# Performance work log

Hardware: AMD Instinct MI355X
Metric: run time of the kernel (lower is better)

The kernel has to match this reference:

```python
import jax, jax.numpy as jnp
import numpy as np

N = 100000      # nodes
E = 1600000     # edges (avg degree 16)
F_DIM = 64      # input feature
H = 64          # hidden1
D1 = 64         # decoder1
P = 200000      # number of query pairs
EPS = 0.0       # GIN eps (train_eps=False)


def setup_inputs() -> dict:
    key = jax.random.key(0)
    ks = jax.random.split(key, 12)
    x = jax.random.normal(ks[0], (N, F_DIM), jnp.float32)
    edge_index = jax.random.randint(ks[1], (2, E), 0, N, dtype=jnp.int32)
    curvature = jax.random.normal(ks[2], (E,), jnp.float32)
    idx = jax.random.randint(ks[3], (2, P), 0, N, dtype=jnp.int32)
    s1 = 1.0 / np.sqrt(F_DIM)
    s2 = 1.0 / np.sqrt(H)
    s3 = 1.0 / np.sqrt(4 * H)
    s4 = 1.0 / np.sqrt(D1)
    w1 = jax.random.uniform(ks[4], (F_DIM, H), jnp.float32, -s1, s1)
    b1 = jax.random.uniform(ks[5], (H,), jnp.float32, -s1, s1)
    w2 = jax.random.uniform(ks[6], (H, H), jnp.float32, -s2, s2)
    b2 = jax.random.uniform(ks[7], (H,), jnp.float32, -s2, s2)
    dw1 = jax.random.uniform(ks[8], (4 * H, D1), jnp.float32, -s3, s3)
    db1 = jax.random.uniform(ks[9], (D1,), jnp.float32, -s3, s3)
    dw2 = jax.random.uniform(ks[10], (D1, 1), jnp.float32, -s4, s4)
    db2 = jax.random.uniform(ks[11], (1,), jnp.float32, -s4, s4)
    return {"x": x, "edge_index": edge_index, "curvature": curvature, "idx": idx,
            "w1": w1, "b1": b1, "w2": w2, "b2": b2,
            "dw1": dw1, "db1": db1, "dw2": dw2, "db2": db2}


def reference(x, edge_index, curvature, idx, w1, b1, w2, b2, dw1, db1, dw2, db2):
    # curvature path: abs + dropout (eval mode => identity), result unused by output
    _ = jnp.abs(curvature)
    src, dst = edge_index[0], edge_index[1]
    # GIN aggregation with self-loops of weight 1: sum_j x_j + x_i
    agg = jax.ops.segment_sum(x[src], dst, num_segments=N) + x  # [N, F]
    h = (1.0 + EPS) * x + agg
    # nn = Linear -> ReLU -> Linear
    h = jnp.maximum(h @ w1 + b1, 0.0) @ w2 + b2                 # [N, H]
    h = jnp.maximum(h, 0.0)                                     # outer ReLU
    e1 = h[idx[0]]                                              # [P, H]
    e2 = h[idx[1]]                                              # [P, H]
    feat = jnp.concatenate([e1 + e2, e1 * e2, e1, e2], axis=1)  # [P, 4H]
    log = jnp.maximum(feat @ dw1 + db1, 0.0) @ dw2 + db2        # [P, 1]
    return log
```

## Files before the change

### kernel.cpp

```cpp
#include <hip/hip_runtime.h>
#include <hip/hip_bf16.h>
#include <hip/hip_fp16.h>
#include <cstdint>

#define N_NODES 100000
#define N_EDGES 1600000
#define FDIM 64
#define NPAIRS 200000
#define NB 391
#define BCAP 4864
#define SSTR 5632
#define EPB 6250

typedef __attribute__((ext_vector_type(8))) short short8;
typedef __attribute__((ext_vector_type(8))) _Float16 half8;
typedef __attribute__((ext_vector_type(4))) float floatx4;

__device__ __forceinline__ unsigned short bf16_rtne(float f) {
    unsigned u = __float_as_uint(f);
    unsigned r = (u + 0x7fffu + ((u >> 16) & 1u)) >> 16;
    return (unsigned short)r;
}

__device__ __forceinline__ void split8_rtne(const float* f, short8& hi, short8& lo) {
#pragma unroll
    for (int j = 0; j < 8; ++j) {
        unsigned short h = bf16_rtne(f[j]);
        hi[j] = (short)h;
        float hf = __uint_as_float(((unsigned)h) << 16);
        lo[j] = (short)bf16_rtne(f[j] - hf);
    }
}

__device__ __forceinline__ void split8_trunc(const float* f, short8& hi, short8& lo) {
#pragma unroll
    for (int j = 0; j < 8; ++j) {
        unsigned u = __float_as_uint(f[j]);
        hi[j] = (short)(unsigned short)(u >> 16);
        float hf = __uint_as_float(u & 0xffff0000u);
        float r = f[j] - hf;
        lo[j] = (short)(unsigned short)(__float_as_uint(r) >> 16);
    }
}

__global__ void k0_init(const float4* __restrict__ x4, float4* __restrict__ h04,
                        __half* __restrict__ xh, int* __restrict__ ovfFlag) {
    int i = blockIdx.x * blockDim.x + threadIdx.x;
    if (i == 0) ovfFlag[0] = 0;
    if (i < N_NODES * FDIM / 4) {
        float4 v = x4[i];
        float4 d = {2.f * v.x, 2.f * v.y, 2.f * v.z, 2.f * v.w};
        h04[i] = d;
        ushort4 o;
        o.x = __half_as_ushort(__float2half(v.x));
        o.y = __half_as_ushort(__float2half(v.y));
        o.z = __half_as_ushort(__float2half(v.z));
        o.w = __half_as_ushort(__float2half(v.w));
        ((ushort4*)xh)[i] = o;
    }
}

__global__ void __launch_bounds__(256) p1a_hist(const int* __restrict__ dst,
                                                int* __restrict__ matrix) {
    __shared__ int hist[NB];
    int tid = threadIdx.x, blk = blockIdx.x;
    for (int i = tid; i < NB; i += 256) hist[i] = 0;
    __syncthreads();
    int base = blk * EPB;
    for (int i = tid; i < EPB; i += 256) {
        int d = dst[base + i];
        atomicAdd(&hist[d >> 8], 1);
    }
    __syncthreads();
    for (int i = tid; i < NB; i += 256) matrix[blk * NB + i] = hist[i];
}

__global__ void __launch_bounds__(256) p1b_scan(int* __restrict__ matrix,
                                                int* __restrict__ bucketCnt) {
    __shared__ int s[256];
    int b = blockIdx.x, t = threadIdx.x;
    int v = matrix[t * NB + b];
    s[t] = v;
    __syncthreads();
    for (int off = 1; off < 256; off <<= 1) {
        int u = (t >= off) ? s[t - off] : 0;
        __syncthreads();
        s[t] += u;
        __syncthreads();
    }
    matrix[t * NB + b] = s[t] - v;
    if (t == 255) bucketCnt[b] = s[255];
}

__global__ void __launch_bounds__(256) p1c_scatter(const int* __restrict__ src,
        const int* __restrict__ dst, const float* __restrict__ x,
        float* __restrict__ h0, const int* __restrict__ matrix,
        int* __restrict__ bucketArr, int* __restrict__ ovfFlag) {
    __shared__ int cur[NB];
    int tid = threadIdx.x, blk = blockIdx.x;
    for (int i = tid; i < NB; i += 256) cur[i] = matrix[blk * NB + i];
    __syncthreads();
    int base = blk * EPB;
    for (int i = tid; i < EPB; i += 256) {
        int e = base + i;
        int s = src[e], d = dst[e];
        int b = d >> 8;
        int pos = atomicAdd(&cur[b], 1);
        if (pos < BCAP) {
            bucketArr[(size_t)b * SSTR + pos] = ((d & 255) << 17) | s;
        } else {
            atomicOr(ovfFlag, 1);
            const float* xr = x + (size_t)s * FDIM;
            float* hr = h0 + (size_t)d * FDIM;
            for (int f = 0; f < FDIM; ++f) atomicAdd(&hr[f], xr[f]);
        }
    }
}

__global__ void __launch_bounds__(256) p2_build(int* __restrict__ bucketArr,
        const int* __restrict__ bucketCnt, int* __restrict__ rowptr,
        int* __restrict__ deg) {
    __shared__ int ebuf[BCAP];
    __shared__ int hist[256], sc[256], cur[256];
    int b = blockIdx.x, t = threadIdx.x;
    int cnt = bucketCnt[b];
    if (cnt > BCAP) cnt = BCAP;
    int* arr = bucketArr + (size_t)b * SSTR;
    hist[t] = 0;
    __syncthreads();
    for (int i = t; i < cnt; i += 256) {
        int e = arr[i];
        ebuf[i] = e;
        atomicAdd(&hist[(e >> 17) & 255], 1);
    }
    __syncthreads();
    int h = hist[t];
    int pc = (h + 3) & ~3;
    sc[t] = pc;
    __syncthreads();
    for (int off = 1; off < 256; off <<= 1) {
        int u = (t >= off) ? sc[t - off] : 0;
        __syncthreads();
        sc[t] += u;
        __syncthreads();
    }
    int rbase = sc[t] - pc;
    cur[t] = rbase;
    int n = (b << 8) + t;
    if (n < N_NODES) {
        rowptr[n] = b * SSTR + rbase;
        deg[n] = h;
    }
    __syncthreads();
    for (int i = t; i < cnt; i += 256) {
        int e = ebuf[i];
        int dl = (e >> 17) & 255;
        int pos = atomicAdd(&cur[dl], 1);
        arr[pos] = e & 0x1FFFF;
    }
}

__device__ __forceinline__ void addrow(float4& acc, const __half* __restrict__ xh,
                                       int s, int fq) {
    float2 raw = *(const float2*)(xh + (size_t)s * 64 + fq * 4);
    __half2 a = *(__half2*)&raw.x;
    __half2 b = *(__half2*)&raw.y;
    float2 fa = __half22float2(a);
    float2 fb = __half22float2(b);
    acc.x += fa.x; acc.y += fa.y; acc.z += fb.x; acc.w += fb.y;
}

__global__ void __launch_bounds__(256) k2_agg(const __half* __restrict__ xh,
                       float4* __restrict__ h04, const int* __restrict__ deg,
                       const int* __restrict__ rowptr, const int* __restrict__ csr,
                       const int* __restrict__ ovfFlag) {
    int gid = blockIdx.x * 256 + threadIdx.x;
    int n = gid >> 4, fq = gid & 15;
    int dc = deg[n];
    const int4* srow = (const int4*)(csr + rowptr[n]);
    float4 acc;
    if (ovfFlag[0]) {
        acc = h04[(size_t)n * 16 + fq];
    } else {
        float2 raw = *(const float2*)(xh + (size_t)n * 64 + fq * 4);
        __half2 a = *(__half2*)&raw.x;
        __half2 b = *(__half2*)&raw.y;
        float2 fa = __half22float2(a);
        float2 fb = __half22float2(b);
        acc = (float4){2.f * fa.x, 2.f * fa.y, 2.f * fb.x, 2.f * fb.y};
    }
    for (int i = 0; i < dc; i += 16) {
        int4 s4 = srow[i >> 2];
        int4 s5, s6, s7;
        if (i + 4 < dc)  s5 = srow[(i >> 2) + 1];
        if (i + 8 < dc)  s6 = srow[(i >> 2) + 2];
        if (i + 12 < dc) s7 = srow[(i >> 2) + 3];
        addrow(acc, xh, s4.x, fq);
        if (i + 1 < dc)  addrow(acc, xh, s4.y, fq);
        if (i + 2 < dc)  addrow(acc, xh, s4.z, fq);
        if (i + 3 < dc)  addrow(acc, xh, s4.w, fq);
        if (i + 4 < dc)  addrow(acc, xh, s5.x, fq);
        if (i + 5 < dc)  addrow(acc, xh, s5.y, fq);
        if (i + 6 < dc)  addrow(acc, xh, s5.z, fq);
        if (i + 7 < dc)  addrow(acc, xh, s5.w, fq);
        if (i + 8 < dc)  addrow(acc, xh, s6.x, fq);
        if (i + 9 < dc)  addrow(acc, xh, s6.y, fq);
        if (i + 10 < dc) addrow(acc, xh, s6.z, fq);
        if (i + 11 < dc) addrow(acc, xh, s6.w, fq);
        if (i + 12 < dc) addrow(acc, xh, s7.x, fq);
        if (i + 13 < dc) addrow(acc, xh, s7.y, fq);
        if (i + 14 < dc) addrow(acc, xh, s7.z, fq);
        if (i + 15 < dc) addrow(acc, xh, s7.w, fq);
    }
    h04[(size_t)n * 16 + fq] = acc;
}

__global__ void __launch_bounds__(256) k3_mfma(const float* __restrict__ h,
        __half* __restrict__ hh,
        const float* __restrict__ w1, const float* __restrict__ b1,
        const float* __restrict__ w2, const float* __restrict__ b2) {
    __shared__ short8 W1H[512], W1L[512], W2H[512], W2L[512];
    __shared__ float Tbuf[4 * 16 * 68];
    int tid = threadIdx.x;
    for (int f = tid; f < 512; f += 256) {
        int flane = f & 63, st = f >> 6;
        int t = st & 3, s = st >> 2;
        int fq = flane >> 4, fp = flane & 15;
        int n = t * 16 + fp;
        int K0 = s * 32 + fq * 8;
        float wv[8];
#pragma unroll
        for (int j = 0; j < 8; ++j) wv[j] = w1[(K0 + j) * 64 + n];
        short8 hi, lo;
        split8_rtne(wv, hi, lo);
        W1H[f] = hi; W1L[f] = lo;
#pragma unroll
        for (int j = 0; j < 8; ++j) wv[j] = w2[(K0 + j) * 64 + n];
        split8_rtne(wv, hi, lo);
        W2H[f] = hi; W2L[f] = lo;
    }
    __syncthreads();
    int lane = tid & 63;
    int q = lane >> 4, p = lane & 15;
    int wtid0 = blockIdx.x * 4 + (tid >> 6);
    int wtid = wtid0 < 6249 ? wtid0 : 6249;
    int n0 = wtid * 16;
    float b1t[4], b2t[4];
#pragma unroll
    for (int t = 0; t < 4; ++t) {
        b1t[t] = b1[t * 16 + p];
        b2t[t] = b2[t * 16 + p];
    }
    const float* hrow = h + (size_t)(n0 + p) * 64;
    float4 a0 = *(const float4*)(hrow + q * 8);
    float4 a1 = *(const float4*)(hrow + q * 8 + 4);
    float4 a2 = *(const float4*)(hrow + 32 + q * 8);
    float4 a3 = *(const float4*)(hrow + 32 + q * 8 + 4);
    float f0[8] = {a0.x, a0.y, a0.z, a0.w, a1.x, a1.y, a1.z, a1.w};
    float f1[8] = {a2.x, a2.y, a2.z, a2.w, a3.x, a3.y, a3.z, a3.w};
    short8 Ah0, Al0, Ah1, Al1;
    split8_trunc(f0, Ah0, Al0);
    split8_trunc(f1, Ah1, Al1);
    floatx4 acc[4];
#pragma unroll
    for (int t = 0; t < 4; ++t) acc[t] = (floatx4){0.f, 0.f, 0.f, 0.f};
#pragma unroll
    for (int t = 0; t < 4; ++t) {
        short8 bh = W1H[t * 64 + lane], bl = W1L[t * 64 + lane];
        acc[t] = __builtin_amdgcn_mfma_f32_16x16x32_bf16(Ah0, bh, acc[t], 0, 0, 0);
        acc[t] = __builtin_amdgcn_mfma_f32_16x16x32_bf16(Al0, bh, acc[t], 0, 0, 0);
        acc[t] = __builtin_amdgcn_mfma_f32_16x16x32_bf16(Ah0, bl, acc[t], 0, 0, 0);
        bh = W1H[(4 + t) * 64 + lane]; bl = W1L[(4 + t) * 64 + lane];
        acc[t] = __builtin_amdgcn_mfma_f32_16x16x32_bf16(Ah1, bh, acc[t], 0, 0, 0);
        acc[t] = __builtin_amdgcn_mfma_f32_16x16x32_bf16(Al1, bh, acc[t], 0, 0, 0);
        acc[t] = __builtin_amdgcn_mfma_f32_16x16x32_bf16(Ah1, bl, acc[t], 0, 0, 0);
    }
    float* T = Tbuf + (tid >> 6) * (16 * 68);
#pragma unroll
    for (int t = 0; t < 4; ++t) {
#pragma unroll
        for (int r = 0; r < 4; ++r)
            T[(q * 4 + r) * 68 + t * 16 + p] = fmaxf(acc[t][r] + b1t[t], 0.f);
    }
    const float* Tp = T + p * 68;
    float4 u0 = *(const float4*)(Tp + q * 8);
    float4 u1 = *(const float4*)(Tp + q * 8 + 4);
    float4 u2 = *(const float4*)(Tp + 32 + q * 8);
    float4 u3 = *(const float4*)(Tp + 32 + q * 8 + 4);
    float g0[8] = {u0.x, u0.y, u0.z, u0.w, u1.x, u1.y, u1.z, u1.w};
    float g1[8] = {u2.x, u2.y, u2.z, u2.w, u3.x, u3.y, u3.z, u3.w};
    split8_trunc(g0, Ah0, Al0);
    split8_trunc(g1, Ah1, Al1);
#pragma unroll
    for (int t = 0; t < 4; ++t) acc[t] = (floatx4){0.f, 0.f, 0.f, 0.f};
#pragma unroll
    for (int t = 0; t < 4; ++t) {
        short8 bh = W2H[t * 64 + lane], bl = W2L[t * 64 + lane];
        acc[t] = __builtin_amdgcn_mfma_f32_16x16x32_bf16(Ah0, bh, acc[t], 0, 0, 0);
        acc[t] = __builtin_amdgcn_mfma_f32_16x16x32_bf16(Al0, bh, acc[t], 0, 0, 0);
        acc[t] = __builtin_amdgcn_mfma_f32_16x16x32_bf16(Ah0, bl, acc[t], 0, 0, 0);
        bh = W2H[(4 + t) * 64 + lane]; bl = W2L[(4 + t) * 64 + lane];
        acc[t] = __builtin_amdgcn_mfma_f32_16x16x32_bf16(Ah1, bh, acc[t], 0, 0, 0);
        acc[t] = __builtin_amdgcn_mfma_f32_16x16x32_bf16(Al1, bh, acc[t], 0, 0, 0);
        acc[t] = __builtin_amdgcn_mfma_f32_16x16x32_bf16(Ah1, bl, acc[t], 0, 0, 0);
    }
    if (wtid0 < 6250) {
#pragma unroll
        for (int t = 0; t < 4; ++t) {
#pragma unroll
            for (int r = 0; r < 4; ++r)
                hh[(size_t)(n0 + q * 4 + r) * 64 + t * 16 + p] =
                    __float2half(fmaxf(acc[t][r] + b2t[t], 0.f));
        }
    }
}

__global__ void __launch_bounds__(256) k4_pair(const __half* __restrict__ hh,
                        const int* __restrict__ qidx,
                        const float* __restrict__ dw1, const float* __restrict__ db1,
                        const float* __restrict__ dw2, const float* __restrict__ db2,
                        float* __restrict__ out, int numWaves) {
    __shared__ half8 BF[2048];
    int tid = threadIdx.x;
    for (int f = tid; f < 2048; f += 256) {
        int lane = f & 63, st = f >> 6;
        int t = st & 3, s = st >> 2;
        int q = lane >> 4, nl = lane & 15;
        int n = t * 16 + nl;
        int K0 = s * 32 + q * 8;
        half8 hv;
#pragma unroll
        for (int j = 0; j < 8; ++j) hv[j] = (_Float16)dw1[(K0 + j) * 64 + n];
        BF[f] = hv;
    }
    __syncthreads();
    int lane = tid & 63;
    int q = lane >> 4, nl = lane & 15;
    float db1t[4], dw2t[4];
#pragma unroll
    for (int t = 0; t < 4; ++t) {
        db1t[t] = db1[t * 16 + nl];
        dw2t[t] = dw2[t * 16 + nl];
    }
    float db2v = db2[0];
    int wid = (blockIdx.x * 256 + tid) >> 6;
    for (int task = wid; task < NPAIRS / 16; task += numWaves) {
        int p0 = task * 16;
        int i1 = qidx[p0 + nl];
        int i2 = qidx[NPAIRS + p0 + nl];
        const half8* r1 = (const half8*)(hh + (size_t)i1 * 64);
        const half8* r2 = (const half8*)(hh + (size_t)i2 * 64);
        half8 e1a = r1[q],     e1b = r1[4 + q];
        half8 e2a = r2[q],     e2b = r2[4 + q];
        half8 sA = e1a + e2a,  sB = e1b + e2b;
        half8 pA = e1a * e2a,  pB = e1b * e2b;
        floatx4 acc[4];
#pragma unroll
        for (int t = 0; t < 4; ++t) acc[t] = (floatx4){0.f, 0.f, 0.f, 0.f};

#define DO_STEP(S, AV)                                                        \
        _Pragma("unroll")                                                     \
        for (int t = 0; t < 4; ++t)                                           \
            acc[t] = __builtin_amdgcn_mfma_f32_16x16x32_f16(                  \
                (AV), BF[((S) * 4 + t) * 64 + lane], acc[t], 0, 0, 0);

        DO_STEP(0, sA)
        DO_STEP(1, sB)
        DO_STEP(2, pA)
        DO_STEP(3, pB)
        DO_STEP(4, e1a)
        DO_STEP(5, e1b)
        DO_STEP(6, e2a)
        DO_STEP(7, e2b)
#undef DO_STEP

        float part[4] = {0.f, 0.f, 0.f, 0.f};
#pragma unroll
        for (int t = 0; t < 4; ++t) {
#pragma unroll
            for (int r = 0; r < 4; ++r)
                part[r] = fmaf(fmaxf(acc[t][r] + db1t[t], 0.f), dw2t[t], part[r]);
        }
#pragma unroll
        for (int off = 1; off < 16; off <<= 1) {
#pragma unroll
            for (int r = 0; r < 4; ++r) part[r] += __shfl_xor(part[r], off, 64);
        }
        if (nl == 0) {
#pragma unroll
            for (int r = 0; r < 4; ++r) out[p0 + q * 4 + r] = part[r] + db2v;
        }
    }
}

extern "C" void kernel_launch(void* const* d_in, const int* in_sizes, int n_in,
                              void* d_out, int out_size, void* d_ws, size_t ws_size,
                              hipStream_t stream) {
    const float* x    = (const float*)d_in[0];
    const int*   eidx = (const int*)d_in[1];
    const int*   qidx = (const int*)d_in[3];
    const float* w1   = (const float*)d_in[4];
    const float* b1   = (const float*)d_in[5];
    const float* w2   = (const float*)d_in[6];
    const float* b2   = (const float*)d_in[7];
    const float* dw1  = (const float*)d_in[8];
    const float* db1  = (const float*)d_in[9];
    const float* dw2  = (const float*)d_in[10];
    const float* db2  = (const float*)d_in[11];
    float* out = (float*)d_out;

    char* ws = (char*)d_ws;
    float*  h0        = (float*)ws;
    __half* xh        = (__half*)(ws + 25600000);
    int*    bucketArr = (int*)(ws + 38400000);
    int*    rowptr    = (int*)(ws + 47208448);
    int*    deg       = (int*)(ws + 47608448);
    int*    matrix    = (int*)(ws + 48008448);
    int*    bucketCnt = (int*)(ws + 48408832);
    int*    ovfFlag   = (int*)(ws + 48410396);

    const int* src = eidx;
    const int* dst = eidx + N_EDGES;

    k0_init<<<6250, 256, 0, stream>>>((const float4*)x, (float4*)h0, xh, ovfFlag);
    p1a_hist<<<256, 256, 0, stream>>>(dst, matrix);
    p1b_scan<<<NB, 256, 0, stream>>>(matrix, bucketCnt);
    p1c_scatter<<<256, 256, 0, stream>>>(src, dst, x, h0, matrix, bucketArr,
                                         ovfFlag);
    p2_build<<<NB, 256, 0, stream>>>(bucketArr, bucketCnt, rowptr, deg);
    k2_agg<<<6250, 256, 0, stream>>>(xh, (float4*)h0, deg, rowptr, bucketArr,
                                     ovfFlag);
    k3_mfma<<<1563, 256, 0, stream>>>(h0, xh, w1, b1, w2, b2);
    const int blocks4 = 625;
    k4_pair<<<blocks4, 256, 0, stream>>>(xh, qidx, dw1, db1, dw2, db2, out,
                                         blocks4 * 4);
}
```

Before: 228.4 us.

## Store aggregated features as fp16, use single f16 MFMA, fuse init with histogram

```diff
diff --git a/kernel.cpp b/kernel.cpp
--- a/kernel.cpp
+++ b/kernel.cpp
@@ -12,67 +12,32 @@
 #define SSTR 5632
 #define EPB 6250
 
-typedef __attribute__((ext_vector_type(8))) short short8;
 typedef __attribute__((ext_vector_type(8))) _Float16 half8;
 typedef __attribute__((ext_vector_type(4))) float floatx4;
 
-__device__ __forceinline__ unsigned short bf16_rtne(float f) {
-    unsigned u = __float_as_uint(f);
-    unsigned r = (u + 0x7fffu + ((u >> 16) & 1u)) >> 16;
-    return (unsigned short)r;
-}
-
-__device__ __forceinline__ void split8_rtne(const float* f, short8& hi, short8& lo) {
-#pragma unroll
-    for (int j = 0; j < 8; ++j) {
-        unsigned short h = bf16_rtne(f[j]);
-        hi[j] = (short)h;
-        float hf = __uint_as_float(((unsigned)h) << 16);
-        lo[j] = (short)bf16_rtne(f[j] - hf);
-    }
-}
-
-__device__ __forceinline__ void split8_trunc(const float* f, short8& hi, short8& lo) {
-#pragma unroll
-    for (int j = 0; j < 8; ++j) {
-        unsigned u = __float_as_uint(f[j]);
-        hi[j] = (short)(unsigned short)(u >> 16);
-        float hf = __uint_as_float(u & 0xffff0000u);
-        float r = f[j] - hf;
-        lo[j] = (short)(unsigned short)(__float_as_uint(r) >> 16);
-    }
-}
-
-__global__ void k0_init(const float4* __restrict__ x4, float4* __restrict__ h04,
-                        __half* __restrict__ xh, int* __restrict__ ovfFlag) {
-    int i = blockIdx.x * blockDim.x + threadIdx.x;
-    if (i == 0) ovfFlag[0] = 0;
-    if (i < N_NODES * FDIM / 4) {
-        float4 v = x4[i];
-        float4 d = {2.f * v.x, 2.f * v.y, 2.f * v.z, 2.f * v.w};
-        h04[i] = d;
-        ushort4 o;
-        o.x = __half_as_ushort(__float2half(v.x));
-        o.y = __half_as_ushort(__float2half(v.y));
-        o.z = __half_as_ushort(__float2half(v.z));
-        o.w = __half_as_ushort(__float2half(v.w));
-        ((ushort4*)xh)[i] = o;
-    }
-}
-
-__global__ void __launch_bounds__(256) p1a_hist(const int* __restrict__ dst,
-                                                int* __restrict__ matrix) {
+__global__ void __launch_bounds__(256) k0_fused(const float4* __restrict__ x4,
+        __half* __restrict__ xh, const int* __restrict__ dst,
+        int* __restrict__ matrix, int* __restrict__ ovfCnt) {
     __shared__ int hist[NB];
-    int tid = threadIdx.x, blk = blockIdx.x;
-    for (int i = tid; i < NB; i += 256) hist[i] = 0;
-    __syncthreads();
-    int base = blk * EPB;
-    for (int i = tid; i < EPB; i += 256) {
-        int d = dst[base + i];
-        atomicAdd(&hist[d >> 8], 1);
-    }
-    __syncthreads();
-    for (int i = tid; i < NB; i += 256) matrix[blk * NB + i] = hist[i];
+    int blk = blockIdx.x, tid = threadIdx.x;
+    int i = blk * 256 + tid;
+    if (i == 0) ovfCnt[0] = 0;
+    float4 v = x4[i];
+    ushort4 o;
+    o.x = __half_as_ushort(__float2half(v.x));
+    o.y = __half_as_ushort(__float2half(v.y));
+    o.z = __half_as_ushort(__float2half(v.z));
+    o.w = __half_as_ushort(__float2half(v.w));
+    ((ushort4*)xh)[i] = o;
+    if (blk < 256) {
+        for (int j = tid; j < NB; j += 256) hist[j] = 0;
+        __syncthreads();
+        int base = blk * EPB;
+        for (int j = tid; j < EPB; j += 256)
+            atomicAdd(&hist[dst[base + j] >> 8], 1);
+        __syncthreads();
+        for (int j = tid; j < NB; j += 256) matrix[blk * NB + j] = hist[j];
+    }
 }
 
 __global__ void __launch_bounds__(256) p1b_scan(int* __restrict__ matrix,
@@ -93,9 +58,9 @@
 }
 
 __global__ void __launch_bounds__(256) p1c_scatter(const int* __restrict__ src,
-        const int* __restrict__ dst, const float* __restrict__ x,
-        float* __restrict__ h0, const int* __restrict__ matrix,
-        int* __restrict__ bucketArr, int* __restrict__ ovfFlag) {
+        const int* __restrict__ dst, const int* __restrict__ matrix,
+        int* __restrict__ bucketArr, int* __restrict__ ovfCnt,
+        int2* __restrict__ ovfList) {
     __shared__ int cur[NB];
     int tid = threadIdx.x, blk = blockIdx.x;
     for (int i = tid; i < NB; i += 256) cur[i] = matrix[blk * NB + i];
@@ -109,10 +74,8 @@
         if (pos < BCAP) {
             bucketArr[(size_t)b * SSTR + pos] = ((d & 255) << 17) | s;
         } else {
-            atomicOr(ovfFlag, 1);
-            const float* xr = x + (size_t)s * FDIM;
-            float* hr = h0 + (size_t)d * FDIM;
-            for (int f = 0; f < FDIM; ++f) atomicAdd(&hr[f], xr[f]);
+            int idx = atomicAdd(ovfCnt, 1);
+            ovfList[idx] = make_int2(d, s);
         }
     }
 }
@@ -171,23 +134,30 @@
 }
 
 __global__ void __launch_bounds__(256) k2_agg(const __half* __restrict__ xh,
-                       float4* __restrict__ h04, const int* __restrict__ deg,
+                       __half* __restrict__ h0h, const int* __restrict__ deg,
                        const int* __restrict__ rowptr, const int* __restrict__ csr,
-                       const int* __restrict__ ovfFlag) {
+                       const int* __restrict__ ovfCnt,
+                       const int2* __restrict__ ovfList,
+                       const float* __restrict__ x) {
     int gid = blockIdx.x * 256 + threadIdx.x;
     int n = gid >> 4, fq = gid & 15;
     int dc = deg[n];
     const int4* srow = (const int4*)(csr + rowptr[n]);
-    float4 acc;
-    if (ovfFlag[0]) {
-        acc = h04[(size_t)n * 16 + fq];
-    } else {
-        float2 raw = *(const float2*)(xh + (size_t)n * 64 + fq * 4);
-        __half2 a = *(__half2*)&raw.x;
-        __half2 b = *(__half2*)&raw.y;
-        float2 fa = __half22float2(a);
-        float2 fb = __half22float2(b);
-        acc = (float4){2.f * fa.x, 2.f * fa.y, 2.f * fb.x, 2.f * fb.y};
+    float2 raw = *(const float2*)(xh + (size_t)n * 64 + fq * 4);
+    __half2 sa = *(__half2*)&raw.x;
+    __half2 sb = *(__half2*)&raw.y;
+    float2 fa = __half22float2(sa);
+    float2 fb = __half22float2(sb);
+    float4 acc = {2.f * fa.x, 2.f * fa.y, 2.f * fb.x, 2.f * fb.y};
+    int oc = ovfCnt[0];
+    if (oc > 0) {
+        for (int i = 0; i < oc; ++i) {
+            int2 e = ovfList[i];
+            if (e.x == n) {
+                const float* xr = x + (size_t)e.y * 64 + fq * 4;
+                acc.x += xr[0]; acc.y += xr[1]; acc.z += xr[2]; acc.w += xr[3];
+            }
+        }
     }
     for (int i = 0; i < dc; i += 16) {
         int4 s4 = srow[i >> 2];
@@ -212,32 +182,35 @@
         if (i + 14 < dc) addrow(acc, xh, s7.z, fq);
         if (i + 15 < dc) addrow(acc, xh, s7.w, fq);
     }
-    h04[(size_t)n * 16 + fq] = acc;
-}
-
-__global__ void __launch_bounds__(256) k3_mfma(const float* __restrict__ h,
-        __half* __restrict__ hh,
-        const float* __restrict__ w1, const float* __restrict__ b1,
-        const float* __restrict__ w2, const float* __restrict__ b2) {
-    __shared__ short8 W1H[512], W1L[512], W2H[512], W2L[512];
+    ushort4 st;
+    st.x = __half_as_ushort(__float2half(acc.x));
+    st.y = __half_as_ushort(__float2half(acc.y));
+    st.z = __half_as_ushort(__float2half(acc.z));
+    st.w = __half_as_ushort(__float2half(acc.w));
+    ((ushort4*)h0h)[(size_t)n * 16 + fq] = st;
+}
+
+__global__ void __launch_bounds__(256) k3_mfma(const __half* __restrict__ h,
+        __half* __restrict__ hh, const float* __restrict__ w1,
+        const float* __restrict__ b1, const float* __restrict__ w2,
+        const float* __restrict__ b2) {
+    __shared__ half8 WF1[512], WF2[512];
     __shared__ float Tbuf[4 * 16 * 68];
     int tid = threadIdx.x;
     for (int f = tid; f < 512; f += 256) {
-        int flane = f & 63, st = f >> 6;
-        int t = st & 3, s = st >> 2;
-        int fq = flane >> 4, fp = flane & 15;
-        int n = t * 16 + fp;
-        int K0 = s * 32 + fq * 8;
-        float wv[8];
-#pragma unroll
-        for (int j = 0; j < 8; ++j) wv[j] = w1[(K0 + j) * 64 + n];
-        short8 hi, lo;
-        split8_rtne(wv, hi, lo);
-        W1H[f] = hi; W1L[f] = lo;
-#pragma unroll
-        for (int j = 0; j < 8; ++j) wv[j] = w2[(K0 + j) * 64 + n];
-        split8_rtne(wv, hi, lo);
-        W2H[f] = hi; W2L[f] = lo;
+        int lane = f & 63, st = f >> 6;
+        int t = st & 3, kh = st >> 2;
+        int q = lane >> 4, nl = lane & 15;
+        int n = t * 16 + nl;
+        int K0 = kh * 32 + q * 8;
+        half8 hv1, hv2;
+#pragma unroll
+        for (int j = 0; j < 8; ++j) {
+            hv1[j] = (_Float16)w1[(K0 + j) * 64 + n];
+            hv2[j] = (_Float16)w2[(K0 + j) * 64 + n];
+        }
+        WF1[f] = hv1;
+        WF2[f] = hv2;
     }
     __syncthreads();
     int lane = tid & 63;
@@ -251,29 +224,17 @@
         b1t[t] = b1[t * 16 + p];
         b2t[t] = b2[t * 16 + p];
     }
-    const float* hrow = h + (size_t)(n0 + p) * 64;
-    float4 a0 = *(const float4*)(hrow + q * 8);
-    float4 a1 = *(const float4*)(hrow + q * 8 + 4);
-    float4 a2 = *(const float4*)(hrow + 32 + q * 8);
-    float4 a3 = *(const float4*)(hrow + 32 + q * 8 + 4);
-    float f0[8] = {a0.x, a0.y, a0.z, a0.w, a1.x, a1.y, a1.z, a1.w};
-    float f1[8] = {a2.x, a2.y, a2.z, a2.w, a3.x, a3.y, a3.z, a3.w};
-    short8 Ah0, Al0, Ah1, Al1;
-    split8_trunc(f0, Ah0, Al0);
-    split8_trunc(f1, Ah1, Al1);
+    const half8* hrow = (const half8*)(h + (size_t)(n0 + p) * 64);
+    half8 A0 = hrow[q], A1 = hrow[4 + q];
     floatx4 acc[4];
 #pragma unroll
     for (int t = 0; t < 4; ++t) acc[t] = (floatx4){0.f, 0.f, 0.f, 0.f};
 #pragma unroll
     for (int t = 0; t < 4; ++t) {
-        short8 bh = W1H[t * 64 + lane], bl = W1L[t * 64 + lane];
-        acc[t] = __builtin_amdgcn_mfma_f32_16x16x32_bf16(Ah0, bh, acc[t], 0, 0, 0);
-        acc[t] = __builtin_amdgcn_mfma_f32_16x16x32_bf16(Al0, bh, acc[t], 0, 0, 0);
-        acc[t] = __builtin_amdgcn_mfma_f32_16x16x32_bf16(Ah0, bl, acc[t], 0, 0, 0);
-        bh = W1H[(4 + t) * 64 + lane]; bl = W1L[(4 + t) * 64 + lane];
-        acc[t] = __builtin_amdgcn_mfma_f32_16x16x32_bf16(Ah1, bh, acc[t], 0, 0, 0);
-        acc[t] = __builtin_amdgcn_mfma_f32_16x16x32_bf16(Al1, bh, acc[t], 0, 0, 0);
-        acc[t] = __builtin_amdgcn_mfma_f32_16x16x32_bf16(Ah1, bl, acc[t], 0, 0, 0);
+        acc[t] = __builtin_amdgcn_mfma_f32_16x16x32_f16(A0, WF1[t * 64 + lane],
+                                                        acc[t], 0, 0, 0);
+        acc[t] = __builtin_amdgcn_mfma_f32_16x16x32_f16(A1, WF1[(4 + t) * 64 + lane],
+                                                        acc[t], 0, 0, 0);
     }
     float* T = Tbuf + (tid >> 6) * (16 * 68);
 #pragma unroll
@@ -287,22 +248,23 @@
     float4 u1 = *(const float4*)(Tp + q * 8 + 4);
     float4 u2 = *(const float4*)(Tp + 32 + q * 8);
     float4 u3 = *(const float4*)(Tp + 32 + q * 8 + 4);
-    float g0[8] = {u0.x, u0.y, u0.z, u0.w, u1.x, u1.y, u1.z, u1.w};
-    float g1[8] = {u2.x, u2.y, u2.z, u2.w, u3.x, u3.y, u3.z, u3.w};
-    split8_trunc(g0, Ah0, Al0);
-    split8_trunc(g1, Ah1, Al1);
+    half8 g0, g1;
+    g0[0] = (_Float16)u0.x; g0[1] = (_Float16)u0.y;
+    g0[2] = (_Float16)u0.z; g0[3] = (_Float16)u0.w;
+    g0[4] = (_Float16)u1.x; g0[5] = (_Float16)u1.y;
+    g0[6] = (_Float16)u1.z; g0[7] = (_Float16)u1.w;
+    g1[0] = (_Float16)u2.x; g1[1] = (_Float16)u2.y;
+    g1[2] = (_Float16)u2.z; g1[3] = (_Float16)u2.w;
+    g1[4] = (_Float16)u3.x; g1[5] = (_Float16)u3.y;
+    g1[6] = (_Float16)u3.z; g1[7] = (_Float16)u3.w;
 #pragma unroll
     for (int t = 0; t < 4; ++t) acc[t] = (floatx4){0.f, 0.f, 0.f, 0.f};
 #pragma unroll
     for (int t = 0; t < 4; ++t) {
-        short8 bh = W2H[t * 64 + lane], bl = W2L[t * 64 + lane];
-        acc[t] = __builtin_amdgcn_mfma_f32_16x16x32_bf16(Ah0, bh, acc[t], 0, 0, 0);
-        acc[t] = __builtin_amdgcn_mfma_f32_16x16x32_bf16(Al0, bh, acc[t], 0, 0, 0);
-        acc[t] = __builtin_amdgcn_mfma_f32_16x16x32_bf16(Ah0, bl, acc[t], 0, 0, 0);
-        bh = W2H[(4 + t) * 64 + lane]; bl = W2L[(4 + t) * 64 + lane];
-        acc[t] = __builtin_amdgcn_mfma_f32_16x16x32_bf16(Ah1, bh, acc[t], 0, 0, 0);
-        acc[t] = __builtin_amdgcn_mfma_f32_16x16x32_bf16(Al1, bh, acc[t], 0, 0, 0);
-        acc[t] = __builtin_amdgcn_mfma_f32_16x16x32_bf16(Ah1, bl, acc[t], 0, 0, 0);
+        acc[t] = __builtin_amdgcn_mfma_f32_16x16x32_f16(g0, WF2[t * 64 + lane],
+                                                        acc[t], 0, 0, 0);
+        acc[t] = __builtin_amdgcn_mfma_f32_16x16x32_f16(g1, WF2[(4 + t) * 64 + lane],
+                                                        acc[t], 0, 0, 0);
     }
     if (wtid0 < 6250) {
 #pragma unroll
@@ -410,27 +372,27 @@
     float* out = (float*)d_out;
 
     char* ws = (char*)d_ws;
-    float*  h0        = (float*)ws;
-    __half* xh        = (__half*)(ws + 25600000);
-    int*    bucketArr = (int*)(ws + 38400000);
+    __half* h0h       = (__half*)ws;
+    __half* xh        = (__half*)(ws + 12800000);
+    int*    bucketArr = (int*)(ws + 25600000);
+    int2*   ovfList   = (int2*)(ws + 34408448);
     int*    rowptr    = (int*)(ws + 47208448);
     int*    deg       = (int*)(ws + 47608448);
     int*    matrix    = (int*)(ws + 48008448);
     int*    bucketCnt = (int*)(ws + 48408832);
-    int*    ovfFlag   = (int*)(ws + 48410396);
+    int*    ovfCnt    = (int*)(ws + 48410396);
 
     const int* src = eidx;
     const int* dst = eidx + N_EDGES;
 
-    k0_init<<<6250, 256, 0, stream>>>((const float4*)x, (float4*)h0, xh, ovfFlag);
-    p1a_hist<<<256, 256, 0, stream>>>(dst, matrix);
+    k0_fused<<<6250, 256, 0, stream>>>((const float4*)x, xh, dst, matrix, ovfCnt);
     p1b_scan<<<NB, 256, 0, stream>>>(matrix, bucketCnt);
-    p1c_scatter<<<256, 256, 0, stream>>>(src, dst, x, h0, matrix, bucketArr,
-                                         ovfFlag);
+    p1c_scatter<<<256, 256, 0, stream>>>(src, dst, matrix, bucketArr,
+                                         ovfCnt, ovfList);
     p2_build<<<NB, 256, 0, stream>>>(bucketArr, bucketCnt, rowptr, deg);
-    k2_agg<<<6250, 256, 0, stream>>>(xh, (float4*)h0, deg, rowptr, bucketArr,
-                                     ovfFlag);
-    k3_mfma<<<1563, 256, 0, stream>>>(h0, xh, w1, b1, w2, b2);
+    k2_agg<<<6250, 256, 0, stream>>>(xh, h0h, deg, rowptr, bucketArr,
+                                     ovfCnt, ovfList, x);
+    k3_mfma<<<1563, 256, 0, stream>>>(h0h, xh, w1, b1, w2, b2);
     const int blocks4 = 625;
     k4_pair<<<blocks4, 256, 0, stream>>>(xh, qidx, dw1, db1, dw2, db2, out,
                                          blocks4 * 4);
```

After: 215.6 us. 5.6% less time.
